# Kernel tuning notes

Hardware: AMD Instinct MI355X
Metric: run time of the kernel (lower is better)

The kernel has to match this reference:

```python
import jax, jax.numpy as jnp
import numpy as np

ALPHA = 0.7
GAMMA = 0.2
INF = 1e9


def setup_inputs() -> dict:
    key = jax.random.key(0)
    k1, k2 = jax.random.split(key)
    B, T, C = 64, 1024, 8
    pred = jax.random.normal(k1, (B, T, C), dtype=jnp.float32)
    target = jax.random.normal(k2, (B, T, C), dtype=jnp.float32)
    return {"pred": pred, "target": target}


def _soft_dtw(pred, target, gamma):
    # pred, target: [B, T, C]; squared-Euclidean pairwise cost D: [B, T, T]
    B, T, _ = pred.shape
    x2 = jnp.sum(pred * pred, axis=-1)          # [B, T]
    y2 = jnp.sum(target * target, axis=-1)      # [B, T]
    D = x2[:, :, None] + y2[:, None, :] - 2.0 * jnp.einsum('btc,bsc->bts', pred, target)

    i_idx = jnp.arange(T)

    def step(carry, k):
        # anti-diagonal wavefront: diagonal k holds cells (i, k-i)
        r_km2, r_km1 = carry                     # each [B, T], indexed by row i
        j_idx = k - i_idx
        valid = (j_idx >= 0) & (j_idx < T)
        jc = jnp.clip(j_idx, 0, T - 1)
        d_k = D[:, i_idx, jc]                    # [B, T]
        # neighbors: R[i-1, j] and R[i, j-1] on diag k-1; R[i-1, j-1] on diag k-2
        up = jnp.concatenate([jnp.full((B, 1), INF, D.dtype), r_km1[:, :-1]], axis=1)
        left = r_km1
        diag = jnp.concatenate([jnp.full((B, 1), INF, D.dtype), r_km2[:, :-1]], axis=1)
        # virtual origin R[-1,-1] = 0 feeds cell (0,0) on diagonal k == 0
        diag = jnp.where(((k == 0) & (i_idx == 0))[None, :], 0.0, diag)
        stacked = jnp.stack([up, left, diag], axis=0)          # [3, B, T]
        smin = -gamma * jax.nn.logsumexp(-stacked / gamma, axis=0)
        r_new = jnp.where(valid[None, :], d_k + smin, INF)
        return (r_km1, r_new), None

    init = (jnp.full((B, T), INF, D.dtype), jnp.full((B, T), INF, D.dtype))
    (_, r_last), _ = jax.lax.scan(step, init, jnp.arange(2 * T - 1))
    # R[T-1, T-1] sits on the last diagonal at row index T-1
    return jnp.mean(r_last[:, T - 1])


def reference(pred, target):
    mse = jnp.mean((pred - target) ** 2)
    sdtw = _soft_dtw(pred, target, GAMMA)
    return ALPHA * mse + (1.0 - ALPHA) * sdtw
```

## Files before the change

### kernel.cpp

```cpp
#include <hip/hip_runtime.h>


constexpr int TT = 1024;
constexpr float ALPHA_ = 0.7f;
constexpr float FINF = 1000000000.0f;
constexpr int RING = 1088;

__device__ __forceinline__ float shflup1(float old0, float v) {
    return __int_as_float(__builtin_amdgcn_update_dpp(
        __float_as_int(old0), __float_as_int(v), 0x138, 0xf, 0xf, false));
}
__device__ __forceinline__ float rotdn1(float v) {
    return __int_as_float(__builtin_amdgcn_update_dpp(
        0, __float_as_int(v), 0x130, 0xf, 0xf, false));
}

__global__ __launch_bounds__(256) void sdtw_band_kernel(
    const float* __restrict__ pred, const float* __restrict__ target,
    float* __restrict__ ws)
{
    __shared__ float4 s_c4[TT * 3];
    __shared__ float  s_row[4][1088];
    __shared__ float  s_red[4];
    __shared__ int    s_prog[4];

    const int blk = blockIdx.x;
    const int b   = blk & 63;
    const int q   = blk >> 6;
    const int tid = threadIdx.x;
    const int l   = tid & 63;
    const int w_  = __builtin_amdgcn_readfirstlane(tid >> 6);
    const int g   = (q << 2) + w_;
    const int gbase = g << 6;
    const int row   = gbase + l;

    if (tid < 4) s_prog[tid] = -1;

    const float* pr = pred   + ((size_t)b * TT + row) * 8;
    const float* tr = target + ((size_t)b * TT + row) * 8;
    const float4 pa = ((const float4*)pr)[0];
    const float4 pb = ((const float4*)pr)[1];
    const float4 ma = ((const float4*)tr)[0];
    const float4 mb = ((const float4*)tr)[1];

    float x2 = 0.f, msep = 0.f;
    {
        const float pp[8] = {pa.x,pa.y,pa.z,pa.w,pb.x,pb.y,pb.z,pb.w};
        const float tt[8] = {ma.x,ma.y,ma.z,ma.w,mb.x,mb.y,mb.z,mb.w};
        #pragma unroll
        for (int c = 0; c < 8; ++c) {
            x2 = fmaf(pp[c], pp[c], x2);
            float d = pp[c] - tt[c];
            msep = fmaf(d, d, msep);
        }
    }
    const float* tg = target + (size_t)b * TT * 8;
    #pragma unroll
    for (int c0 = 0; c0 < 4; ++c0) {
        const int col = tid + (c0 << 8);
        const float4 u0 = ((const float4*)(tg + (size_t)col * 8))[0];
        const float4 u1 = ((const float4*)(tg + (size_t)col * 8))[1];
        const float y2 = u0.x*u0.x + u0.y*u0.y + u0.z*u0.z + u0.w*u0.w
                       + u1.x*u1.x + u1.y*u1.y + u1.z*u1.z + u1.w*u1.w;
        s_c4[3*col]   = make_float4(-2.f*u0.x, -2.f*u0.y, -2.f*u0.z, -2.f*u0.w);
        s_c4[3*col+1] = make_float4(-2.f*u1.x, -2.f*u1.y, -2.f*u1.z, -2.f*u1.w);
        s_c4[3*col+2] = make_float4(y2, 0.f, 0.f, 0.f);
    }
    #pragma unroll
    for (int off = 32; off > 0; off >>= 1) msep += __shfl_down(msep, off, 64);
    if (l == 0) s_red[w_] = msep;
    __syncthreads();
    if (tid == 0) ws[blk] = s_red[0] + s_red[1] + s_red[2] + s_red[3];

    unsigned long long* rings = (unsigned long long*)(ws + 320);
    unsigned long long* pub = rings + (size_t)(q * 64 + b) * RING;
    unsigned long long* con = rings + (size_t)((q - 1) * 64 + b) * RING;
    const int kb_pub   = 256 * q + 192;
    const int kb_con   = 256 * q - 64;
    const int kmax_con = kb_con + 1086;

    const float c1 = 7.213475204444817f;
    const float c2 = 0.13862943611198906f;
    const int amin = g << 2;
    const int amax = amin + 67;
    const int prodmax = amin + 63;

    float r1 = FINF;
    float dgp;
    unsigned long long pe1 = 0;
    int ppf = 0;
    float hpf1 = 0.f;
    int hpff = 0;
    float hv;

    {
        float hvd0;
        if (w_ == 0) {
            if (q == 0) {
                hvd0 = (l == 0) ? 0.0f : FINF;
            } else {
                const int kk2 = (amin << 4) - 2 + l;
                const int id2 = min(kk2 - kb_con, RING - 1);
                const bool n2 = (l < 16) && (kk2 <= kmax_con);
                unsigned long long e2;
                do {
                    e2 = __hip_atomic_load(con + id2, __ATOMIC_RELAXED,
                                           __HIP_MEMORY_SCOPE_AGENT);
                } while (!__all((!n2) | ((int)(e2 >> 32) == kk2)));
                hvd0 = n2 ? __uint_as_float((unsigned)e2) : FINF;
            }
        } else {
            const int need0 = (amin < prodmax) ? amin : prodmax;
            int pv;
            do {
                pv = __hip_atomic_load(&s_prog[w_ - 1], __ATOMIC_ACQUIRE,
                                       __HIP_MEMORY_SCOPE_WORKGROUP);
            } while (pv < need0);
            hvd0 = s_row[w_ - 1][min(62 + l, 1087)];
        }
        dgp = shflup1(hvd0, FINF);
    }

#define STEPF(i, BA,BB,BY, CA,CB,CY, DCI, DC2, RH) do {                     \
        const float up_ = shflup1(hv, r1);                                  \
        hv = rotdn1(hv);                                                    \
        const int j_ = jb1 + (i);                                           \
        BA = s_c4[3*j_]; BB = s_c4[3*j_+1]; BY = s_c4[3*j_+2].x;            \
        float m_, M_;                                                       \
        asm("v_min3_f32 %0, %1, %2, %3"                                     \
            : "=v"(m_) : "v"(up_), "v"(r1), "v"(dgp));                      \
        asm("v_max3_f32 %0, %1, %2, %3"                                     \
            : "=v"(M_) : "v"(up_), "v"(r1), "v"(dgp));                      \
        const float md_ = __builtin_amdgcn_fmed3f(up_, r1, dgp);            \
        dgp = up_;                                                          \
        const float mc_ = m_ * c1;                                          \
        const float ea_ = __builtin_amdgcn_exp2f(fmaf(md_, -c1, mc_));      \
        const float eb_ = __builtin_amdgcn_exp2f(fmaf(M_,  -c1, mc_));      \
        {   float ac_ = x2 + CY, ac2_ = 0.f;                                \
            ac_  = fmaf(pa.x, CA.x, ac_ );  ac2_ = fmaf(pa.y, CA.y, ac2_);  \
            ac_  = fmaf(pa.z, CA.z, ac_ );  ac2_ = fmaf(pa.w, CA.w, ac2_);  \
            ac_  = fmaf(pb.x, CB.x, ac_ );  ac2_ = fmaf(pb.y, CB.y, ac2_);  \
            ac_  = fmaf(pb.z, CB.z, ac_ );  ac2_ = fmaf(pb.w, CB.w, ac2_);  \
            DC2 = ac_ + ac2_; }                                             \
        const float lg_ = __builtin_amdgcn_logf(1.0f + (ea_ + eb_));        \
        const float rn_ = (DCI) + fmaf(-c2, lg_, m_);                       \
        r1 = rn_; RH = rn_;                                                 \
    } while (0)

#define STEPF0(i, BA,BB,BY, DCI, RH) do {                                   \
        const float up_ = shflup1(hv, r1);                                  \
        hv = rotdn1(hv);                                                    \
        const int j_ = jb1 + (i);                                           \
        BA = s_c4[3*j_]; BB = s_c4[3*j_+1]; BY = s_c4[3*j_+2].x;            \
        float m_, M_;                                                       \
        asm("v_min3_f32 %0, %1, %2, %3"                                     \
            : "=v"(m_) : "v"(up_), "v"(r1), "v"(dgp));                      \
        asm("v_max3_f32 %0, %1, %2, %3"                                     \
            : "=v"(M_) : "v"(up_), "v"(r1), "v"(dgp));                      \
        const float md_ = __builtin_amdgcn_fmed3f(up_, r1, dgp);            \
        dgp = up_;                                                          \
        const float mc_ = m_ * c1;                                          \
        const float ea_ = __builtin_amdgcn_exp2f(fmaf(md_, -c1, mc_));      \
        const float eb_ = __builtin_amdgcn_exp2f(fmaf(M_,  -c1, mc_));      \
        const float lg_ = __builtin_amdgcn_logf(1.0f + (ea_ + eb_));        \
        const float rn_ = (DCI) + fmaf(-c2, lg_, m_);                       \
        r1 = rn_; RH = rn_;                                                 \
    } while (0)

#define DMATHT(CA,CB,CY, DC2) do {                                          \
        float ac_ = x2 + CY, ac2_ = 0.f;                                    \
        ac_  = fmaf(pa.x, CA.x, ac_ );  ac2_ = fmaf(pa.y, CA.y, ac2_);      \
        ac_  = fmaf(pa.z, CA.z, ac_ );  ac2_ = fmaf(pa.w, CA.w, ac2_);      \
        ac_  = fmaf(pb.x, CB.x, ac_ );  ac2_ = fmaf(pb.y, CB.y, ac2_);      \
        ac_  = fmaf(pb.z, CB.z, ac_ );  ac2_ = fmaf(pb.w, CB.w, ac2_);      \
        DC2 = ac_ + ac2_;                                                   \
    } while (0)

#define STEPE(i, DCI, RH) do {                                              \
        const float up_ = shflup1(hv, r1);                                  \
        hv = rotdn1(hv);                                                    \
        float m_, M_;                                                       \
        asm("v_min3_f32 %0, %1, %2, %3"                                     \
            : "=v"(m_) : "v"(up_), "v"(r1), "v"(dgp));                      \
        asm("v_max3_f32 %0, %1, %2, %3"                                     \
            : "=v"(M_) : "v"(up_), "v"(r1), "v"(dgp));                      \
        const float md_ = __builtin_amdgcn_fmed3f(up_, r1, dgp);            \
        dgp = up_;                                                          \
        const float mc_ = m_ * c1;                                          \
        const float ea_ = __builtin_amdgcn_exp2f(fmaf(md_, -c1, mc_));      \
        const float eb_ = __builtin_amdgcn_exp2f(fmaf(M_,  -c1, mc_));      \
        const float lg_ = __builtin_amdgcn_logf(1.0f + (ea_ + eb_));        \
        float rn_ = (DCI) + fmaf(-c2, lg_, m_);                             \
        rn_ = ((unsigned)(jb0 + (i)) < (unsigned)TT) ? rn_ : FINF;          \
        r1 = rn_; RH = rn_;                                                 \
    } while (0)

#define DCLAMP(JB, i, DC) do {                                              \
        int jc_ = (JB) + (i);                                               \
        jc_ = jc_ < 0 ? 0 : (jc_ > (TT-1) ? (TT-1) : jc_);                  \
        const float4 va_ = s_c4[3*jc_];                                     \
        const float4 vb_ = s_c4[3*jc_+1];                                   \
        const float  yv_ = s_c4[3*jc_+2].x;                                 \
        float ac_ = x2 + yv_, ac2_ = 0.f;                                   \
        ac_  = fmaf(pa.x, va_.x, ac_ );  ac2_ = fmaf(pa.y, va_.y, ac2_);    \
        ac_  = fmaf(pa.z, va_.z, ac_ );  ac2_ = fmaf(pa.w, va_.w, ac2_);    \
        ac_  = fmaf(pb.x, vb_.x, ac_ );  ac2_ = fmaf(pb.y, vb_.y, ac2_);    \
        ac_  = fmaf(pb.z, vb_.z, ac_ );  ac2_ = fmaf(pb.w, vb_.w, ac2_);    \
        DC = ac_ + ac2_;                                                    \
    } while (0)

    float Dc0,Dc1,Dc2,Dc3,Dc4,Dc5,Dc6,Dc7;
    float Dc8,Dc9,Dc10,Dc11,Dc12,Dc13,Dc14,Dc15;
    {
        const int jb = -l;
        DCLAMP(jb, 0,Dc0 ); DCLAMP(jb, 1,Dc1 ); DCLAMP(jb, 2,Dc2 );
        DCLAMP(jb, 3,Dc3 ); DCLAMP(jb, 4,Dc4 ); DCLAMP(jb, 5,Dc5 );
        DCLAMP(jb, 6,Dc6 ); DCLAMP(jb, 7,Dc7 ); DCLAMP(jb, 8,Dc8 );
        DCLAMP(jb, 9,Dc9 ); DCLAMP(jb,10,Dc10); DCLAMP(jb,11,Dc11);
        DCLAMP(jb,12,Dc12); DCLAMP(jb,13,Dc13); DCLAMP(jb,14,Dc14);
        DCLAMP(jb,15,Dc15);
    }
    float rh14_last = FINF;
    float4 vA0, vB0, vA1, vB1, vA2, vB2;
    float  yv0, yv1, yv2;

    for (int u = 0; u <= 67; ++u) {
        const int a  = amin + u;
        const int k0 = a << 4;
        const int jb0 = (u << 4) - l;
        const int jb1 = jb0 + 16;

        if (w_ == 0) {
            if (q == 0) {
                hv = FINF;
            } else {
                const int kk1 = k0 - 1 + l;
                const int id1 = min(kk1 - kb_con, RING - 1);
                const bool n1 = (l < 16) && (kk1 <= kmax_con);
                unsigned long long e1;
                if (ppf) { e1 = pe1; ppf = 0; }
                else {
                    e1 = __hip_atomic_load(con + id1, __ATOMIC_RELAXED,
                                           __HIP_MEMORY_SCOPE_AGENT);
                }
                while (!__all((!n1) | ((int)(e1 >> 32) == kk1))) {
                    e1 = __hip_atomic_load(con + id1, __ATOMIC_RELAXED,
                                           __HIP_MEMORY_SCOPE_AGENT);
                }
                hv = n1 ? __uint_as_float((unsigned)e1) : FINF;
            }
        } else {
            if (hpff) { hv = hpf1; hpff = 0; }
            else {
                const int need = (a < prodmax) ? a : prodmax;
                int pv;
                do {
                    pv = __hip_atomic_load(&s_prog[w_ - 1], __ATOMIC_ACQUIRE,
                                           __HIP_MEMORY_SCOPE_WORKGROUP);
                } while (pv < need);
                hv = s_row[w_ - 1][min((u << 4) + 63 + l, 1087)];
            }
        }

        float rh0,rh1,rh2,rh3,rh4,rh5,rh6,rh7;
        float rh8,rh9,rh10,rh11,rh12,rh13,rh14,rh15;

        if (u >= 4 && u <= 62) {
            STEPF0( 0, vA0,vB0,yv0,               Dc0 , rh0 );
            STEPF0( 1, vA1,vB1,yv1,               Dc1 , rh1 );
            STEPF ( 2, vA2,vB2,yv2, vA0,vB0,yv0,  Dc2 , Dc0 , rh2 );
            STEPF ( 3, vA0,vB0,yv0, vA1,vB1,yv1,  Dc3 , Dc1 , rh3 );
            STEPF ( 4, vA1,vB1,yv1, vA2,vB2,yv2,  Dc4 , Dc2 , rh4 );
            STEPF ( 5, vA2,vB2,yv2, vA0,vB0,yv0,  Dc5 , Dc3 , rh5 );
            STEPF ( 6, vA0,vB0,yv0, vA1,vB1,yv1,  Dc6 , Dc4 , rh6 );
            STEPF ( 7, vA1,vB1,yv1, vA2,vB2,yv2,  Dc7 , Dc5 , rh7 );
            STEPF ( 8, vA2,vB2,yv2, vA0,vB0,yv0,  Dc8 , Dc6 , rh8 );
            STEPF ( 9, vA0,vB0,yv0, vA1,vB1,yv1,  Dc9 , Dc7 , rh9 );
            STEPF (10, vA1,vB1,yv1, vA2,vB2,yv2,  Dc10, Dc8 , rh10);
            STEPF (11, vA2,vB2,yv2, vA0,vB0,yv0,  Dc11, Dc9 , rh11);
            STEPF (12, vA0,vB0,yv0, vA1,vB1,yv1,  Dc12, Dc10, rh12);
            STEPF (13, vA1,vB1,yv1, vA2,vB2,yv2,  Dc13, Dc11, rh13);
            STEPF (14, vA2,vB2,yv2, vA0,vB0,yv0,  Dc14, Dc12, rh14);
            STEPF (15, vA0,vB0,yv0, vA1,vB1,yv1,  Dc15, Dc13, rh15);
            DMATHT(vA2,vB2,yv2, Dc14);
            DMATHT(vA0,vB0,yv0, Dc15);
        } else {
            STEPE( 0,Dc0 ,rh0 ); STEPE( 1,Dc1 ,rh1 );
            STEPE( 2,Dc2 ,rh2 ); STEPE( 3,Dc3 ,rh3 );
            STEPE( 4,Dc4 ,rh4 ); STEPE( 5,Dc5 ,rh5 );
            STEPE( 6,Dc6 ,rh6 ); STEPE( 7,Dc7 ,rh7 );
            STEPE( 8,Dc8 ,rh8 ); STEPE( 9,Dc9 ,rh9 );
            STEPE(10,Dc10,rh10); STEPE(11,Dc11,rh11);
            STEPE(12,Dc12,rh12); STEPE(13,Dc13,rh13);
            STEPE(14,Dc14,rh14); STEPE(15,Dc15,rh15);
            if (u < 67) {
                DCLAMP(jb1, 0,Dc0 ); DCLAMP(jb1, 1,Dc1 ); DCLAMP(jb1, 2,Dc2 );
                DCLAMP(jb1, 3,Dc3 ); DCLAMP(jb1, 4,Dc4 ); DCLAMP(jb1, 5,Dc5 );
                DCLAMP(jb1, 6,Dc6 ); DCLAMP(jb1, 7,Dc7 ); DCLAMP(jb1, 8,Dc8 );
                DCLAMP(jb1, 9,Dc9 ); DCLAMP(jb1,10,Dc10); DCLAMP(jb1,11,Dc11);
                DCLAMP(jb1,12,Dc12); DCLAMP(jb1,13,Dc13); DCLAMP(jb1,14,Dc14);
                DCLAMP(jb1,15,Dc15);
            } else {
                rh14_last = rh14;
            }
        }

        if (l == 63) {
            float4* dst = (float4*)&s_row[w_][u << 4];
            dst[0] = make_float4(rh0,  rh1,  rh2,  rh3);
            dst[1] = make_float4(rh4,  rh5,  rh6,  rh7);
            dst[2] = make_float4(rh8,  rh9,  rh10, rh11);
            dst[3] = make_float4(rh12, rh13, rh14, rh15);
        }

        if (w_ < 3 && l == 0) {
            __hip_atomic_store(&s_prog[w_], a, __ATOMIC_RELEASE,
                               __HIP_MEMORY_SCOPE_WORKGROUP);
        }
        if (w_ == 3 && q < 3) {
            if (l < 16) {
                const int kk = k0 + l;
                const unsigned long long ev =
                    ((unsigned long long)(unsigned)kk << 32) |
                    (unsigned long long)__float_as_uint(s_row[3][(u << 4) + l]);
                __hip_atomic_store(pub + (kk - kb_pub), ev,
                                   __ATOMIC_RELAXED, __HIP_MEMORY_SCOPE_AGENT);
            }
        }
        if (w_ == 0 && q > 0 && a < amax) {
            const int kk1 = k0 + 15 + l;
            pe1 = __hip_atomic_load(con + min(kk1 - kb_con, RING - 1),
                                    __ATOMIC_RELAXED, __HIP_MEMORY_SCOPE_AGENT);
            ppf = 1;
        }
        if (w_ != 0 && a < amax) {
            const int neednx = ((a + 1) < prodmax) ? (a + 1) : prodmax;
            const int pv = __hip_atomic_load(&s_prog[w_ - 1], __ATOMIC_ACQUIRE,
                                             __HIP_MEMORY_SCOPE_WORKGROUP);
            if (pv >= neednx) {
                hpf1 = s_row[w_ - 1][min(((u + 1) << 4) + 63 + l, 1087)];
                hpff = 1;
            }
        }
    }
    if (q == 3 && tid == 255) ws[256 + b] = rh14_last;
#undef STEPF
#undef STEPF0
#undef DMATHT
#undef STEPE
#undef DCLAMP
}

__global__ __launch_bounds__(256) void finalize2_kernel(
    const float* __restrict__ ws, float* __restrict__ out)
{
    __shared__ float sm[4], ss[4];
    const int tid = threadIdx.x, l = tid & 63, w = tid >> 6;
    float m  = ws[tid];
    float sd = (tid < 64) ? ws[256 + tid] : 0.f;
    #pragma unroll
    for (int off = 32; off > 0; off >>= 1) {
        m  += __shfl_down(m,  off, 64);
        sd += __shfl_down(sd, off, 64);
    }
    if (l == 0) { sm[w] = m; ss[w] = sd; }
    __syncthreads();
    if (tid == 0) {
        float M = sm[0] + sm[1] + sm[2] + sm[3];
        float S = ss[0] + ss[1] + ss[2] + ss[3];
        out[0] = ALPHA_ * (M / 524288.0f) + (1.0f - ALPHA_) * (S / 64.0f);
    }
}

extern "C" void kernel_launch(void* const* d_in, const int* in_sizes, int n_in,
                              void* d_out, int out_size, void* d_ws, size_t ws_size,
                              hipStream_t stream) {
    const float* pred   = (const float*)d_in[0];
    const float* target = (const float*)d_in[1];
    float* ws  = (float*)d_ws;
    float* out = (float*)d_out;

    sdtw_band_kernel<<<256, 256, 0, stream>>>(pred, target, ws);
    finalize2_kernel<<<1, 256, 0, stream>>>(ws, out);
}
```

Baseline: 306.9 us.

## Split each batch across two 512-thread blocks instead of four 256-thread blocks

Each batch's wavefront is now handled by two blocks of eight waves each, instead of four blocks of four waves. More of the row-band handoff goes through LDS progress flags inside a block, and only one cross-block ring handoff through global atomics remains per batch. The cost is fewer blocks (128), so fewer CUs are occupied, and LDS use per block grows with the eight row buffers.

```diff
diff --git a/kernel.cpp b/kernel.cpp
--- a/kernel.cpp
+++ b/kernel.cpp
@@ -15,26 +15,26 @@
         0, __float_as_int(v), 0x130, 0xf, 0xf, false));
 }
 
-__global__ __launch_bounds__(256) void sdtw_band_kernel(
+__global__ __launch_bounds__(512) void sdtw_band_kernel(
     const float* __restrict__ pred, const float* __restrict__ target,
     float* __restrict__ ws)
 {
     __shared__ float4 s_c4[TT * 3];
-    __shared__ float  s_row[4][1088];
-    __shared__ float  s_red[4];
-    __shared__ int    s_prog[4];
+    __shared__ float  s_row[8][1088];
+    __shared__ float  s_red[8];
+    __shared__ int    s_prog[8];
 
     const int blk = blockIdx.x;
     const int b   = blk & 63;
-    const int q   = blk >> 6;
+    const int h   = blk >> 6;
     const int tid = threadIdx.x;
     const int l   = tid & 63;
     const int w_  = __builtin_amdgcn_readfirstlane(tid >> 6);
-    const int g   = (q << 2) + w_;
+    const int g   = (h << 3) + w_;
     const int gbase = g << 6;
     const int row   = gbase + l;
 
-    if (tid < 4) s_prog[tid] = -1;
+    if (tid < 8) s_prog[tid] = -1;
 
     const float* pr = pred   + ((size_t)b * TT + row) * 8;
     const float* tr = target + ((size_t)b * TT + row) * 8;
@@ -56,8 +56,8 @@
     }
     const float* tg = target + (size_t)b * TT * 8;
     #pragma unroll
-    for (int c0 = 0; c0 < 4; ++c0) {
-        const int col = tid + (c0 << 8);
+    for (int c0 = 0; c0 < 2; ++c0) {
+        const int col = tid + (c0 << 9);
         const float4 u0 = ((const float4*)(tg + (size_t)col * 8))[0];
         const float4 u1 = ((const float4*)(tg + (size_t)col * 8))[1];
         const float y2 = u0.x*u0.x + u0.y*u0.y + u0.z*u0.z + u0.w*u0.w
@@ -70,19 +70,23 @@
     for (int off = 32; off > 0; off >>= 1) msep += __shfl_down(msep, off, 64);
     if (l == 0) s_red[w_] = msep;
     __syncthreads();
-    if (tid == 0) ws[blk] = s_red[0] + s_red[1] + s_red[2] + s_red[3];
+    if (tid == 0) {
+        float s0 = 0.f;
+        #pragma unroll
+        for (int i = 0; i < 8; ++i) s0 += s_red[i];
+        ws[blk] = s0;
+    }
 
     unsigned long long* rings = (unsigned long long*)(ws + 320);
-    unsigned long long* pub = rings + (size_t)(q * 64 + b) * RING;
-    unsigned long long* con = rings + (size_t)((q - 1) * 64 + b) * RING;
-    const int kb_pub   = 256 * q + 192;
-    const int kb_con   = 256 * q - 64;
-    const int kmax_con = kb_con + 1086;
+    unsigned long long* pub = rings + (size_t)b * RING;
+    unsigned long long* con = rings + (size_t)b * RING;
+    const int kb_pub   = 448;
+    const int kb_con   = 448;
+    const int kmax_con = 448 + 1087;
 
     const float c1 = 7.213475204444817f;
     const float c2 = 0.13862943611198906f;
     const int amin = g << 2;
-    const int amax = amin + 67;
     const int prodmax = amin + 63;
 
     float r1 = FINF;
@@ -96,10 +100,10 @@
     {
         float hvd0;
         if (w_ == 0) {
-            if (q == 0) {
+            if (h == 0) {
                 hvd0 = (l == 0) ? 0.0f : FINF;
             } else {
-                const int kk2 = (amin << 4) - 2 + l;
+                const int kk2 = (g << 6) - 2 + l;
                 const int id2 = min(kk2 - kb_con, RING - 1);
                 const bool n2 = (l < 16) && (kk2 <= kmax_con);
                 unsigned long long e2;
@@ -110,12 +114,11 @@
                 hvd0 = n2 ? __uint_as_float((unsigned)e2) : FINF;
             }
         } else {
-            const int need0 = (amin < prodmax) ? amin : prodmax;
             int pv;
             do {
                 pv = __hip_atomic_load(&s_prog[w_ - 1], __ATOMIC_ACQUIRE,
                                        __HIP_MEMORY_SCOPE_WORKGROUP);
-            } while (pv < need0);
+            } while (pv < amin);
             hvd0 = s_row[w_ - 1][min(62 + l, 1087)];
         }
         dgp = shflup1(hvd0, FINF);
@@ -231,7 +234,7 @@
         const int jb1 = jb0 + 16;
 
         if (w_ == 0) {
-            if (q == 0) {
+            if (h == 0) {
                 hv = FINF;
             } else {
                 const int kk1 = k0 - 1 + l;
@@ -313,27 +316,27 @@
             dst[3] = make_float4(rh12, rh13, rh14, rh15);
         }
 
-        if (w_ < 3 && l == 0) {
+        if (w_ < 7 && l == 0) {
             __hip_atomic_store(&s_prog[w_], a, __ATOMIC_RELEASE,
                                __HIP_MEMORY_SCOPE_WORKGROUP);
         }
-        if (w_ == 3 && q < 3) {
+        if (w_ == 7 && h == 0) {
             if (l < 16) {
                 const int kk = k0 + l;
                 const unsigned long long ev =
                     ((unsigned long long)(unsigned)kk << 32) |
-                    (unsigned long long)__float_as_uint(s_row[3][(u << 4) + l]);
+                    (unsigned long long)__float_as_uint(s_row[7][(u << 4) + l]);
                 __hip_atomic_store(pub + (kk - kb_pub), ev,
                                    __ATOMIC_RELAXED, __HIP_MEMORY_SCOPE_AGENT);
             }
         }
-        if (w_ == 0 && q > 0 && a < amax) {
+        if (w_ == 0 && h == 1 && u < 67) {
             const int kk1 = k0 + 15 + l;
             pe1 = __hip_atomic_load(con + min(kk1 - kb_con, RING - 1),
                                     __ATOMIC_RELAXED, __HIP_MEMORY_SCOPE_AGENT);
             ppf = 1;
         }
-        if (w_ != 0 && a < amax) {
+        if (w_ != 0 && u < 67) {
             const int neednx = ((a + 1) < prodmax) ? (a + 1) : prodmax;
             const int pv = __hip_atomic_load(&s_prog[w_ - 1], __ATOMIC_ACQUIRE,
                                              __HIP_MEMORY_SCOPE_WORKGROUP);
@@ -343,7 +346,7 @@
             }
         }
     }
-    if (q == 3 && tid == 255) ws[256 + b] = rh14_last;
+    if (h == 1 && tid == 511) ws[256 + b] = rh14_last;
 #undef STEPF
 #undef STEPF0
 #undef DMATHT
@@ -356,7 +359,7 @@
 {
     __shared__ float sm[4], ss[4];
     const int tid = threadIdx.x, l = tid & 63, w = tid >> 6;
-    float m  = ws[tid];
+    float m  = (tid < 128) ? ws[tid] : 0.f;
     float sd = (tid < 64) ? ws[256 + tid] : 0.f;
     #pragma unroll
     for (int off = 32; off > 0; off >>= 1) {
@@ -380,6 +383,6 @@
     float* ws  = (float*)d_ws;
     float* out = (float*)d_out;
 
-    sdtw_band_kernel<<<256, 256, 0, stream>>>(pred, target, ws);
+    sdtw_band_kernel<<<128, 512, 0, stream>>>(pred, target, ws);
     finalize2_kernel<<<1, 256, 0, stream>>>(ws, out);
 }
```

Result: slower. 368.5 us (+20.1%).
